# Kernel tuning notes

Hardware: AMD Instinct MI355X
Metric: run time of the kernel (lower is better)

Reference implementation:

```python
import jax, jax.numpy as jnp
import numpy as np

B, N, MODEL_D = 2, 1024, 2048
KQ_D, V_D, H, I = 128, 128, 8, 4
ROPE_THETA = 10000.0


def _rope(x, theta):
    # x: [b, n, ..., d]; positions along axis 1, rotation over last dim d.
    d = x.shape[-1]
    n = x.shape[1]
    inv_freq = theta ** (-jnp.arange(0, d, 2, dtype=jnp.float32) / d)  # [d/2]
    ang = jnp.arange(n, dtype=jnp.float32)[:, None] * inv_freq          # [n, d/2]
    bshape = (1, n) + (1,) * (x.ndim - 3) + (d // 2,)
    cos = jnp.cos(ang).reshape(bshape).astype(x.dtype)
    sin = jnp.sin(ang).reshape(bshape).astype(x.dtype)
    x1, x2 = jnp.split(x, 2, axis=-1)
    return jnp.concatenate([x1 * cos - x2 * sin, x1 * sin + x2 * cos], axis=-1)


def setup_inputs() -> dict:
    key = jax.random.key(0)
    kx, kq, kk, kv, ko = jax.random.split(key, 5)
    s_in = 1.0 / np.sqrt(MODEL_D)
    s_out = 1.0 / np.sqrt(H * I * V_D)
    x = jax.random.normal(kx, (B, N, MODEL_D), jnp.float32)
    Wq = jax.random.normal(kq, (MODEL_D, H, I, KQ_D), jnp.float32) * s_in
    Wk = jax.random.normal(kk, (MODEL_D, H, KQ_D), jnp.float32) * s_in
    Wv = jax.random.normal(kv, (MODEL_D, H, V_D), jnp.float32) * s_in
    Wo = jax.random.normal(ko, (H, I, V_D, MODEL_D), jnp.float32) * s_out
    return {"x": x, "Wq": Wq, "Wk": Wk, "Wv": Wv, "Wo": Wo}


def reference(x, Wq, Wk, Wv, Wo):
    # GQA projections (per Ueajsum specs)
    q = jnp.einsum('bnd,dhik->bnhik', x, Wq)   # [B,N,H,I,K]
    k = jnp.einsum('bnd,dhc->bnhc', x, Wk)     # [B,N,H,K]
    v = jnp.einsum('bnd,dhv->bnhv', x, Wv)     # [B,N,H,V]
    # RoPE on q and k
    q = _rope(q, ROPE_THETA)
    k = _rope(k, ROPE_THETA)
    # Causal softmax attention, each kv head serves I query heads
    scale = 1.0 / np.sqrt(KQ_D)
    scores = jnp.einsum('bnhic,bmhc->bhinm', q, k) * scale  # [B,H,I,N,N]
    n = x.shape[1]
    causal = jnp.tril(jnp.ones((n, n), dtype=bool))
    scores = jnp.where(causal, scores, jnp.finfo(scores.dtype).min)
    p = jax.nn.softmax(scores, axis=-1)
    out = jnp.einsum('bhinm,bmhv->bnhiv', p, v)              # [B,N,H,I,V]
    return jnp.einsum('bnhiv,hivd->bnd', out, Wo)            # [B,N,D]
```

## Files before the change

kernel.cpp:

```cpp
#include <hip/hip_runtime.h>
#include <hip/hip_bf16.h>

typedef __bf16 bf16x8 __attribute__((ext_vector_type(8)));
typedef float floatx4 __attribute__((ext_vector_type(4)));

static __device__ __forceinline__ void async_cp16(const __bf16* g, __bf16* l) {
    typedef const __attribute__((address_space(1))) unsigned int gu32;
    typedef __attribute__((address_space(3))) unsigned int lu32;
    __builtin_amdgcn_global_load_lds((gu32*)g, (lu32*)l, 16, 0, 0);
}

static __device__ __forceinline__ void tile64_f32(
    const float* __restrict__ src, __bf16* __restrict__ dst,
    int R, int C, int r0, int c0, int tid, __bf16* t )
{
    {
        const int r = tid >> 2, cq = (tid & 3) * 16;
        const float* p = src + (size_t)(r0 + r) * C + c0 + cq;
        float4 f0 = *(const float4*)(p);
        float4 f1 = *(const float4*)(p + 4);
        float4 f2 = *(const float4*)(p + 8);
        float4 f3 = *(const float4*)(p + 12);
        __bf16 v[16] = {
            (__bf16)f0.x, (__bf16)f0.y, (__bf16)f0.z, (__bf16)f0.w,
            (__bf16)f1.x, (__bf16)f1.y, (__bf16)f1.z, (__bf16)f1.w,
            (__bf16)f2.x, (__bf16)f2.y, (__bf16)f2.z, (__bf16)f2.w,
            (__bf16)f3.x, (__bf16)f3.y, (__bf16)f3.z, (__bf16)f3.w };
        #pragma unroll
        for (int e = 0; e < 16; ++e) t[(cq + e) * 72 + r] = v[e];
    }
    __syncthreads();
    {
        const int c = tid >> 2, rq = (tid & 3) * 16;
        uint4 u0 = *(const uint4*)(&t[c * 72 + rq]);
        uint4 u1 = *(const uint4*)(&t[c * 72 + rq + 8]);
        __bf16* q = dst + (size_t)(c0 + c) * R + r0 + rq;
        *(uint4*)(q)     = u0;
        *(uint4*)(q + 8) = u1;
    }
}

static __device__ __forceinline__ void tile64_b16(
    const __bf16* __restrict__ src, __bf16* __restrict__ dst,
    int src_ld, int dst_ld, int tid, __bf16* t )
{
    {
        const int r = tid >> 2, cq = (tid & 3) * 16;
        const __bf16* p = src + (size_t)r * src_ld + cq;
        union { uint4 u; __bf16 b[8]; } a0, a1;
        a0.u = *(const uint4*)(p);
        a1.u = *(const uint4*)(p + 8);
        #pragma unroll
        for (int e = 0; e < 8; ++e) {
            t[(cq + e) * 72 + r]     = a0.b[e];
            t[(cq + 8 + e) * 72 + r] = a1.b[e];
        }
    }
    __syncthreads();
    {
        const int c = tid >> 2, rq = (tid & 3) * 16;
        uint4 u0 = *(const uint4*)(&t[c * 72 + rq]);
        uint4 u1 = *(const uint4*)(&t[c * 72 + rq + 8]);
        __bf16* q = dst + (size_t)c * dst_ld + rq;
        *(uint4*)(q)     = u0;
        *(uint4*)(q + 8) = u1;
    }
}

__global__ __launch_bounds__(256) void prep_kernel(
    const float* __restrict__ x,  __bf16* __restrict__ xb,
    const float* __restrict__ Wq, const float* __restrict__ Wk,
    const float* __restrict__ Wv, __bf16* __restrict__ Wt)
{
    __shared__ __bf16 t[64 * 72];
    const int bk  = blockIdx.x;
    const int tid = threadIdx.x;

    if (bk < 2048) {
        int ct = bk & 63, rt = bk >> 6;
        tile64_f32(Wq, Wt, 2048, 4096, rt * 64, ct * 64, tid, t);
    } else if (bk < 2560) {
        int idx = bk - 2048, ct = idx & 15, rt = idx >> 4;
        tile64_f32(Wk, Wt + (size_t)4096 * 2048, 2048, 1024, rt * 64, ct * 64, tid, t);
    } else if (bk < 3072) {
        int idx = bk - 2560, ct = idx & 15, rt = idx >> 4;
        tile64_f32(Wv, Wt + (size_t)5120 * 2048, 2048, 1024, rt * 64, ct * 64, tid, t);
    } else {
        int idx = (bk - 3072) * 256 + tid;
        const float* p = x + (size_t)idx * 8;
        float4 f0 = *(const float4*)p;
        float4 f1 = *(const float4*)(p + 4);
        union { uint4 u; __bf16 b[8]; } o;
        o.b[0] = (__bf16)f0.x; o.b[1] = (__bf16)f0.y; o.b[2] = (__bf16)f0.z; o.b[3] = (__bf16)f0.w;
        o.b[4] = (__bf16)f1.x; o.b[5] = (__bf16)f1.y; o.b[6] = (__bf16)f1.z; o.b[7] = (__bf16)f1.w;
        *(uint4*)(xb + (size_t)idx * 8) = o.u;
    }
}

__global__ __launch_bounds__(256) void rope_vtrans_wot_kernel(
    __bf16* __restrict__ qkv, __bf16* __restrict__ vt,
    const float* __restrict__ Wo, __bf16* __restrict__ WoT)
{
    __shared__ __bf16 t[64 * 72];
    const int bk  = blockIdx.x;
    const int tid = threadIdx.x;

    if (bk < 2560) {
        int idx  = bk * 256 + tid;
        int part = idx & 7;
        int tt   = idx >> 3;
        int head = tt % 40;
        int row  = tt / 40;
        int n    = row & 1023;
        int col0 = (head < 32) ? head * 128 : 4096 + (head - 32) * 128;
        size_t base = (size_t)row * 6144 + col0 + part * 8;

        union { uint4 u; __bf16 b[8]; } x1, x2, o1, o2;
        x1.u = *(const uint4*)(qkv + base);
        x2.u = *(const uint4*)(qkv + base + 64);
        #pragma unroll
        for (int e = 0; e < 8; ++e) {
            int j = part * 8 + e;
            float inv_freq = exp2f(-(float)j * 0.20762050593046015f);
            float ang = (float)n * inv_freq;
            float sv, cv;
            __sincosf(ang, &sv, &cv);
            float a = (float)x1.b[e], b2 = (float)x2.b[e];
            o1.b[e] = (__bf16)(a * cv - b2 * sv);
            o2.b[e] = (__bf16)(a * sv + b2 * cv);
        }
        *(uint4*)(qkv + base)      = o1.u;
        *(uint4*)(qkv + base + 64) = o2.u;
    } else if (bk < 3072) {
        int idx = bk - 2560;
        int bh = idx >> 5, rem = idx & 31;
        int k0 = (rem >> 1) * 64, v0 = (rem & 1) * 64;
        int b = bh >> 3, h = bh & 7;
        const __bf16* src = qkv + (size_t)(b * 1024 + k0) * 6144 + 5120 + h * 128 + v0;
        __bf16* dst = vt + ((size_t)bh * 128 + v0) * 1024 + k0;
        tile64_b16(src, dst, 6144, 1024, tid, t);
    } else {
        int idx = bk - 3072;
        int ct = idx & 31, rt = idx >> 5;
        tile64_f32(Wo, WoT, 4096, 2048, rt * 64, ct * 64, tid, t);
    }
}

__global__ __launch_bounds__(256) void gemm_bt(
    const __bf16* __restrict__ A,
    const __bf16* __restrict__ Bt,
    __bf16* __restrict__ C,
    int M, int lda, int ldb, int ldc,
    int kc_base, int kc_extra)
{
    __shared__ __bf16 As[128 * 64];
    __shared__ __bf16 Bs[128 * 64];

    const int tid  = threadIdx.x;
    const int wave = tid >> 6;
    const int lane = tid & 63;
    const int quad = lane >> 4;
    const int l15  = lane & 15;
    const int wr   = wave >> 1, wc = wave & 1;

    const int bm = blockIdx.y * 128;
    const int bn = blockIdx.x * 128;
    const int z  = blockIdx.z;
    const int Kc = kc_base + ((z == (int)gridDim.z - 1) ? kc_extra : 0);

    A  += (size_t)z * kc_base;
    Bt += (size_t)z * kc_base;
    C  += (size_t)z * M * ldc;

    floatx4 acc[16];
    #pragma unroll
    for (int i = 0; i < 16; ++i) acc[i] = floatx4{0.f, 0.f, 0.f, 0.f};

    const int sr = lane >> 3;
    const int sc = ((lane & 7) ^ sr) * 8;
    const __bf16* a0 = A  + (size_t)(bm + wave * 32 + sr) * lda + sc;
    const __bf16* b0 = Bt + (size_t)(bn + wave * 32 + sr) * ldb + sc;
    __bf16* asd = As + (wave * 32) * 64;
    __bf16* bsd = Bs + (wave * 32) * 64;

    for (int k0 = 0; k0 < Kc; k0 += 64) {
        __syncthreads();
        #pragma unroll
        for (int r = 0; r < 4; ++r) {
            async_cp16(a0 + (size_t)(r * 8) * lda + k0, asd + (r * 8) * 64);
            async_cp16(b0 + (size_t)(r * 8) * ldb + k0, bsd + (r * 8) * 64);
        }
        __syncthreads();

        #pragma unroll
        for (int ko = 0; ko < 2; ++ko) {
            bf16x8 af[4], bf[4];
            #pragma unroll
            for (int t = 0; t < 4; ++t)
                af[t] = *(const bf16x8*)(
                    &As[(wr * 64 + t * 16 + l15) * 64 + (((ko * 4 + quad) ^ (l15 & 7)) * 8)]);
            #pragma unroll
            for (int u = 0; u < 4; ++u)
                bf[u] = *(const bf16x8*)(
                    &Bs[(wc * 64 + u * 16 + l15) * 64 + (((ko * 4 + quad) ^ (l15 & 7)) * 8)]);
            #pragma unroll
            for (int t = 0; t < 4; ++t)
                #pragma unroll
                for (int u = 0; u < 4; ++u)
                    acc[t * 4 + u] = __builtin_amdgcn_mfma_f32_16x16x32_bf16(
                        af[t], bf[u], acc[t * 4 + u], 0, 0, 0);
        }
    }

    #pragma unroll
    for (int t = 0; t < 4; ++t)
        #pragma unroll
        for (int u = 0; u < 4; ++u)
            #pragma unroll
            for (int r = 0; r < 4; ++r) {
                int row = bm + wr * 64 + t * 16 + quad * 4 + r;
                int col = bn + wc * 64 + u * 16 + l15;
                C[(size_t)row * ldc + col] = (__bf16)acc[t * 4 + u][r];
            }
}

__global__ __launch_bounds__(256) void reduce_kernel(
    const __bf16* __restrict__ part, float* __restrict__ out)
{
    int idx = blockIdx.x * 256 + threadIdx.x;
    const size_t S = (size_t)2048 * 2048;
    union { uint4 u; __bf16 b[8]; } p0, p1, p2;
    p0.u = *(const uint4*)(part + (size_t)idx * 8);
    p1.u = *(const uint4*)(part + S + (size_t)idx * 8);
    p2.u = *(const uint4*)(part + 2 * S + (size_t)idx * 8);
    float4 o0, o1;
    o0.x = (float)p0.b[0] + (float)p1.b[0] + (float)p2.b[0];
    o0.y = (float)p0.b[1] + (float)p1.b[1] + (float)p2.b[1];
    o0.z = (float)p0.b[2] + (float)p1.b[2] + (float)p2.b[2];
    o0.w = (float)p0.b[3] + (float)p1.b[3] + (float)p2.b[3];
    o1.x = (float)p0.b[4] + (float)p1.b[4] + (float)p2.b[4];
    o1.y = (float)p0.b[5] + (float)p1.b[5] + (float)p2.b[5];
    o1.z = (float)p0.b[6] + (float)p1.b[6] + (float)p2.b[6];
    o1.w = (float)p0.b[7] + (float)p1.b[7] + (float)p2.b[7];
    *(float4*)(out + (size_t)idx * 8)     = o0;
    *(float4*)(out + (size_t)idx * 8 + 4) = o1;
}

__global__ __launch_bounds__(512, 2) void attn_kernel(
    const __bf16* __restrict__ qkv,
    const __bf16* __restrict__ vt,
    __bf16* __restrict__ ao)
{
    const int PS_LD = 72;
    __shared__ __bf16 Ks[64 * 128];
    __shared__ __bf16 Vs[128 * 64];
    __shared__ __bf16 Ps[8][16 * PS_LD];

    const int tid  = threadIdx.x;
    const int wave = tid >> 6;
    const int lane = tid & 63;
    const int quad = lane >> 4;
    const int l15  = lane & 15;
    const int i    = wave >> 1;
    const int rt   = wave & 1;

    const int pair = blockIdx.x;
    const int bh   = blockIdx.y;
    const int b    = bh >> 3, h = bh & 7;
    const __bf16* vtb = vt + (size_t)bh * 128 * 1024;

    const int keyA = wave * 8 + (lane >> 4);
    const int keyB = keyA + 4;
    const int chA  = (lane & 15) ^ (keyA & 15);
    const int chB  = (lane & 15) ^ (keyB & 15);
    const __bf16* gK0 = qkv + (size_t)(b * 1024 + keyA) * 6144 + 4096 + h * 128 + chA * 8;
    const __bf16* gK1 = qkv + (size_t)(b * 1024 + keyB) * 6144 + 4096 + h * 128 + chB * 8;
    __bf16* lK0 = Ks + (wave * 8) * 128;
    __bf16* lK1 = Ks + (wave * 8 + 4) * 128;

    const int vdA = wave * 16 + (lane >> 3);
    const int vdB = vdA + 8;
    const int cvA = (lane & 7) ^ (vdA & 7);
    const int cvB = (lane & 7) ^ (vdB & 7);
    const __bf16* gV0 = vtb + (size_t)vdA * 1024 + cvA * 8;
    const __bf16* gV1 = vtb + (size_t)vdB * 1024 + cvB * 8;
    __bf16* lV0 = Vs + (wave * 16) * 64;
    __bf16* lV1 = Vs + (wave * 16 + 8) * 64;

    bf16x8 onesf;
    #pragma unroll
    for (int j = 0; j < 8; ++j) onesf[j] = (__bf16)1.0f;

    const float C2 = 0.12751898549f;

    #pragma unroll
    for (int ph = 0; ph < 2; ++ph) {
        const int qt    = ph ? (31 - pair) : pair;
        const int qrow0 = qt * 32 + rt * 16;

        const __bf16* qp = qkv + (size_t)(b * 1024 + qrow0 + l15) * 6144 + (h * 4 + i) * 128;
        bf16x8 qf[4];
        #pragma unroll
        for (int c = 0; c < 4; ++c)
            qf[c] = *(const bf16x8*)(qp + c * 32 + quad * 8);

        floatx4 acc[8];
        #pragma unroll
        for (int u = 0; u < 8; ++u) acc[u] = floatx4{0.f, 0.f, 0.f, 0.f};
        floatx4 accl = floatx4{0.f, 0.f, 0.f, 0.f};

        const int ntiles = (qt >> 1) + 1;
        for (int t = 0; t < ntiles; ++t) {
            const int kt = t * 64;
            __syncthreads();
            async_cp16(gK0 + (size_t)kt * 6144, lK0);
            async_cp16(gK1 + (size_t)kt * 6144, lK1);
            async_cp16(gV0 + kt, lV0);
            async_cp16(gV1 + kt, lV1);
            __syncthreads();

            floatx4 s[4];
            #pragma unroll
            for (int ks = 0; ks < 4; ++ks) s[ks] = floatx4{0.f, 0.f, 0.f, 0.f};
            #pragma unroll
            for (int c = 0; c < 4; ++c) {
                #pragma unroll
                for (int ks = 0; ks < 4; ++ks) {
                    bf16x8 kf = *(const bf16x8*)(
                        &Ks[(ks * 16 + l15) * 128 + ((c * 4 + quad) ^ l15) * 8]);
                    s[ks] = __builtin_amdgcn_mfma_f32_16x16x32_bf16(qf[c], kf, s[ks], 0, 0, 0);
                }
            }

            #pragma unroll
            for (int r = 0; r < 4; ++r) {
                int qrow = qrow0 + quad * 4 + r;
                #pragma unroll
                for (int ks = 0; ks < 4; ++ks) {
                    int kc = kt + ks * 16 + l15;
                    float p = (kc <= qrow) ? exp2f(s[ks][r] * C2) : 0.0f;
                    Ps[wave][(quad * 4 + r) * PS_LD + ks * 16 + l15] = (__bf16)p;
                }
            }

            #pragma unroll
            for (int s2 = 0; s2 < 2; ++s2) {
                bf16x8 pa = *(const bf16x8*)(&Ps[wave][l15 * PS_LD + s2 * 32 + quad * 8]);
                accl = __builtin_amdgcn_mfma_f32_16x16x32_bf16(pa, onesf, accl, 0, 0, 0);
                #pragma unroll
                for (int u = 0; u < 8; ++u) {
                    bf16x8 vf = *(const bf16x8*)(
                        &Vs[(u * 16 + l15) * 64 + (((s2 * 4 + quad) ^ (l15 & 7))) * 8]);
                    acc[u] = __builtin_amdgcn_mfma_f32_16x16x32_bf16(pa, vf, acc[u], 0, 0, 0);
                }
            }
        }

        #pragma unroll
        for (int r = 0; r < 4; ++r) {
            float inv = 1.0f / accl[r];
            int row = qrow0 + quad * 4 + r;
            __bf16* op = ao + (size_t)(b * 1024 + row) * 4096 + (h * 4 + i) * 128;
            #pragma unroll
            for (int u = 0; u < 8; ++u)
                op[u * 16 + l15] = (__bf16)(acc[u][r] * inv);
        }
    }
}

extern "C" void kernel_launch(void* const* d_in, const int* in_sizes, int n_in,
                              void* d_out, int out_size, void* d_ws, size_t ws_size,
                              hipStream_t stream)
{
    const float* x  = (const float*)d_in[0];
    const float* Wq = (const float*)d_in[1];
    const float* Wk = (const float*)d_in[2];
    const float* Wv = (const float*)d_in[3];
    const float* Wo = (const float*)d_in[4];
    float* out = (float*)d_out;

    const size_t MB = 1024 * 1024;
    char* ws = (char*)d_ws;
    __bf16* qkv  = (__bf16*)(ws);
    __bf16* vtb  = (__bf16*)(ws + 24 * MB);
    __bf16* xb   = (__bf16*)(ws + 28 * MB);
    __bf16* Wt   = (__bf16*)(ws + 36 * MB);
    __bf16* WoT  = (__bf16*)(ws + 28 * MB);
    __bf16* ao   = (__bf16*)(ws + 44 * MB);
    __bf16* part = (__bf16*)(ws);

    prep_kernel<<<5120, 256, 0, stream>>>(x, xb, Wq, Wk, Wv, Wt);
    gemm_bt<<<dim3(48, 16), 256, 0, stream>>>(xb, Wt, qkv, 2048, 2048, 2048, 6144, 2048, 0);
    rope_vtrans_wot_kernel<<<5120, 256, 0, stream>>>(qkv, vtb, Wo, WoT);
    attn_kernel<<<dim3(16, 16), 512, 0, stream>>>(qkv, vtb, ao);
    gemm_bt<<<dim3(16, 16, 3), 256, 0, stream>>>(ao, WoT, part, 2048, 4096, 4096, 2048, 1344, 64);
    reduce_kernel<<<2048, 256, 0, stream>>>(part, out);
}
```

Measured before the change: 295.5 us.

## Rework bf16 GEMM into 256x256 ping-pong pipelined tiles with 512 threads

The shared GEMM now uses 256x256 output tiles computed by 8 waves, with double-buffered LDS. The next K-slice's A and B tiles are prefetched asynchronously across four interleaved MFMA phases, separated by barriers and s_setprio. The goal is to overlap global-to-LDS copies with matrix math and to reuse each loaded tile more. The cost is fewer blocks (192 for both GEMMs), which leaves some CUs idle. Each block also needs 128KB of LDS and many accumulator registers, so occupancy is limited to one block per CU.

```diff
diff --git a/kernel.cpp b/kernel.cpp
--- a/kernel.cpp
+++ b/kernel.cpp
@@ -146,82 +146,190 @@
     }
 }
 
-__global__ __launch_bounds__(256) void gemm_bt(
+__global__ __launch_bounds__(512) void gemm_bt(
     const __bf16* __restrict__ A,
     const __bf16* __restrict__ Bt,
     __bf16* __restrict__ C,
     int M, int lda, int ldb, int ldc,
     int kc_base, int kc_extra)
 {
-    __shared__ __bf16 As[128 * 64];
-    __shared__ __bf16 Bs[128 * 64];
+    __shared__ __bf16 As[2][256 * 64];
+    __shared__ __bf16 Bs[2][256 * 64];
 
     const int tid  = threadIdx.x;
     const int wave = tid >> 6;
     const int lane = tid & 63;
     const int quad = lane >> 4;
     const int l15  = lane & 15;
-    const int wr   = wave >> 1, wc = wave & 1;
-
-    const int bm = blockIdx.y * 128;
-    const int bn = blockIdx.x * 128;
+    const int wr   = wave >> 2;
+    const int wc   = wave & 3;
+
+    const int bm = blockIdx.y * 256;
+    const int bn = blockIdx.x * 256;
     const int z  = blockIdx.z;
     const int Kc = kc_base + ((z == (int)gridDim.z - 1) ? kc_extra : 0);
+    const int NT = Kc >> 6;
 
     A  += (size_t)z * kc_base;
     Bt += (size_t)z * kc_base;
     C  += (size_t)z * M * ldc;
 
-    floatx4 acc[16];
+    floatx4 acc[32];
     #pragma unroll
-    for (int i = 0; i < 16; ++i) acc[i] = floatx4{0.f, 0.f, 0.f, 0.f};
+    for (int i = 0; i < 32; ++i) acc[i] = floatx4{0.f, 0.f, 0.f, 0.f};
 
     const int sr = lane >> 3;
     const int sc = ((lane & 7) ^ sr) * 8;
-    const __bf16* a0 = A  + (size_t)(bm + wave * 32 + sr) * lda + sc;
-    const __bf16* b0 = Bt + (size_t)(bn + wave * 32 + sr) * ldb + sc;
-    __bf16* asd = As + (wave * 32) * 64;
-    __bf16* bsd = Bs + (wave * 32) * 64;
-
-    for (int k0 = 0; k0 < Kc; k0 += 64) {
-        __syncthreads();
-        #pragma unroll
-        for (int r = 0; r < 4; ++r) {
-            async_cp16(a0 + (size_t)(r * 8) * lda + k0, asd + (r * 8) * 64);
-            async_cp16(b0 + (size_t)(r * 8) * ldb + k0, bsd + (r * 8) * 64);
-        }
-        __syncthreads();
-
-        #pragma unroll
-        for (int ko = 0; ko < 2; ++ko) {
-            bf16x8 af[4], bf[4];
-            #pragma unroll
-            for (int t = 0; t < 4; ++t)
-                af[t] = *(const bf16x8*)(
-                    &As[(wr * 64 + t * 16 + l15) * 64 + (((ko * 4 + quad) ^ (l15 & 7)) * 8)]);
-            #pragma unroll
-            for (int u = 0; u < 4; ++u)
-                bf[u] = *(const bf16x8*)(
-                    &Bs[(wc * 64 + u * 16 + l15) * 64 + (((ko * 4 + quad) ^ (l15 & 7)) * 8)]);
-            #pragma unroll
-            for (int t = 0; t < 4; ++t)
-                #pragma unroll
-                for (int u = 0; u < 4; ++u)
-                    acc[t * 4 + u] = __builtin_amdgcn_mfma_f32_16x16x32_bf16(
-                        af[t], bf[u], acc[t * 4 + u], 0, 0, 0);
-        }
-    }
+    const __bf16* a0 = A  + (size_t)(bm + wave * 8 + sr) * lda + sc;
+    const __bf16* b0 = Bt + (size_t)(bn + wave * 8 + sr) * ldb + sc;
+    const int ldsw = wave * 512;
+
+    const int arow = (wr * 128 + l15) * 64;
+    const int brow = (wc * 64  + l15) * 64;
+    const int cx0  = ((0 + quad) ^ (l15 & 7)) * 8;
+    const int cx1  = ((4 + quad) ^ (l15 & 7)) * 8;
 
     #pragma unroll
-    for (int t = 0; t < 4; ++t)
-        #pragma unroll
-        for (int u = 0; u < 4; ++u)
-            #pragma unroll
-            for (int r = 0; r < 4; ++r) {
-                int row = bm + wr * 64 + t * 16 + quad * 4 + r;
-                int col = bn + wc * 64 + u * 16 + l15;
-                C[(size_t)row * ldc + col] = (__bf16)acc[t * 4 + u][r];
-            }
+    for (int q = 0; q < 4; ++q)
+        async_cp16(a0 + (size_t)(q * 64) * lda, (__bf16*)&As[0][q * 4096 + ldsw]);
+    #pragma unroll
+    for (int q = 0; q < 4; ++q)
+        async_cp16(b0 + (size_t)(q * 64) * ldb, (__bf16*)&Bs[0][q * 4096 + ldsw]);
+    if (NT > 1) {
+        #pragma unroll
+        for (int q = 0; q < 4; ++q)
+            async_cp16(b0 + (size_t)(q * 64) * ldb + 64, (__bf16*)&Bs[1][q * 4096 + ldsw]);
+        asm volatile("s_waitcnt vmcnt(4)" ::: "memory");
+    } else {
+        asm volatile("s_waitcnt vmcnt(0)" ::: "memory");
+    }
+    __builtin_amdgcn_s_barrier();
+    __builtin_amdgcn_sched_barrier(0);
+
+    for (int t = 0; t < NT; ++t) {
+        const int cur = t & 1;
+        const __bf16* Ac = As[cur];
+        const __bf16* Bc = Bs[cur];
+        __bf16* An = (__bf16*)As[cur ^ 1];
+        __bf16* Bn = (__bf16*)Bs[cur];
+
+        bf16x8 af[4][2], bfA[2][2], bfB[2][2];
+
+        #pragma unroll
+        for (int tt = 0; tt < 4; ++tt) {
+            af[tt][0] = *(const bf16x8*)(&Ac[arow + tt * 1024 + cx0]);
+            af[tt][1] = *(const bf16x8*)(&Ac[arow + tt * 1024 + cx1]);
+        }
+        #pragma unroll
+        for (int uu = 0; uu < 2; ++uu) {
+            bfA[uu][0] = *(const bf16x8*)(&Bc[brow + uu * 1024 + cx0]);
+            bfA[uu][1] = *(const bf16x8*)(&Bc[brow + uu * 1024 + cx1]);
+        }
+        if (t + 1 < NT) {
+            #pragma unroll
+            for (int q = 0; q < 4; ++q)
+                async_cp16(a0 + (size_t)(q * 64) * lda + (t + 1) * 64,
+                           An + q * 4096 + ldsw);
+        }
+        __builtin_amdgcn_s_barrier();
+        asm volatile("s_waitcnt lgkmcnt(0)" ::: "memory");
+        __builtin_amdgcn_sched_barrier(0);
+        __builtin_amdgcn_s_setprio(1);
+        #pragma unroll
+        for (int ko = 0; ko < 2; ++ko)
+            #pragma unroll
+            for (int tt = 0; tt < 4; ++tt)
+                #pragma unroll
+                for (int uu = 0; uu < 2; ++uu)
+                    acc[tt * 4 + uu] = __builtin_amdgcn_mfma_f32_16x16x32_bf16(
+                        af[tt][ko], bfA[uu][ko], acc[tt * 4 + uu], 0, 0, 0);
+        __builtin_amdgcn_s_setprio(0);
+        __builtin_amdgcn_s_barrier();
+        __builtin_amdgcn_sched_barrier(0);
+
+        #pragma unroll
+        for (int uu = 0; uu < 2; ++uu) {
+            bfB[uu][0] = *(const bf16x8*)(&Bc[brow + (2 + uu) * 1024 + cx0]);
+            bfB[uu][1] = *(const bf16x8*)(&Bc[brow + (2 + uu) * 1024 + cx1]);
+        }
+        __builtin_amdgcn_s_barrier();
+        asm volatile("s_waitcnt lgkmcnt(0)" ::: "memory");
+        __builtin_amdgcn_sched_barrier(0);
+        __builtin_amdgcn_s_setprio(1);
+        #pragma unroll
+        for (int ko = 0; ko < 2; ++ko)
+            #pragma unroll
+            for (int tt = 0; tt < 4; ++tt)
+                #pragma unroll
+                for (int uu = 0; uu < 2; ++uu)
+                    acc[tt * 4 + 2 + uu] = __builtin_amdgcn_mfma_f32_16x16x32_bf16(
+                        af[tt][ko], bfB[uu][ko], acc[tt * 4 + 2 + uu], 0, 0, 0);
+        __builtin_amdgcn_s_setprio(0);
+        __builtin_amdgcn_s_barrier();
+        __builtin_amdgcn_sched_barrier(0);
+
+        #pragma unroll
+        for (int tt = 0; tt < 4; ++tt) {
+            af[tt][0] = *(const bf16x8*)(&Ac[arow + (4 + tt) * 1024 + cx0]);
+            af[tt][1] = *(const bf16x8*)(&Ac[arow + (4 + tt) * 1024 + cx1]);
+        }
+        if (t + 2 < NT) {
+            #pragma unroll
+            for (int q = 0; q < 2; ++q)
+                async_cp16(b0 + (size_t)(q * 64) * ldb + (t + 2) * 64,
+                           Bn + q * 4096 + ldsw);
+        }
+        __builtin_amdgcn_s_barrier();
+        asm volatile("s_waitcnt lgkmcnt(0)" ::: "memory");
+        __builtin_amdgcn_sched_barrier(0);
+        __builtin_amdgcn_s_setprio(1);
+        #pragma unroll
+        for (int ko = 0; ko < 2; ++ko)
+            #pragma unroll
+            for (int tt = 0; tt < 4; ++tt)
+                #pragma unroll
+                for (int uu = 0; uu < 2; ++uu)
+                    acc[(4 + tt) * 4 + uu] = __builtin_amdgcn_mfma_f32_16x16x32_bf16(
+                        af[tt][ko], bfA[uu][ko], acc[(4 + tt) * 4 + uu], 0, 0, 0);
+        __builtin_amdgcn_s_setprio(0);
+        __builtin_amdgcn_s_barrier();
+        __builtin_amdgcn_sched_barrier(0);
+
+        if (t + 2 < NT) {
+            #pragma unroll
+            for (int q = 2; q < 4; ++q)
+                async_cp16(b0 + (size_t)(q * 64) * ldb + (t + 2) * 64,
+                           Bn + q * 4096 + ldsw);
+        }
+        __builtin_amdgcn_s_setprio(1);
+        #pragma unroll
+        for (int ko = 0; ko < 2; ++ko)
+            #pragma unroll
+            for (int tt = 0; tt < 4; ++tt)
+                #pragma unroll
+                for (int uu = 0; uu < 2; ++uu)
+                    acc[(4 + tt) * 4 + 2 + uu] = __builtin_amdgcn_mfma_f32_16x16x32_bf16(
+                        af[tt][ko], bfB[uu][ko], acc[(4 + tt) * 4 + 2 + uu], 0, 0, 0);
+        __builtin_amdgcn_s_setprio(0);
+        if (t + 2 < NT) {
+            asm volatile("s_waitcnt vmcnt(4)" ::: "memory");
+        } else {
+            asm volatile("s_waitcnt vmcnt(0)" ::: "memory");
+        }
+        __builtin_amdgcn_s_barrier();
+        __builtin_amdgcn_sched_barrier(0);
+    }
+
+    #pragma unroll
+    for (int tt = 0; tt < 8; ++tt)
+        #pragma unroll
+        for (int uu = 0; uu < 4; ++uu) {
+            const int row = bm + wr * 128 + tt * 16 + quad * 4;
+            const int col = bn + wc * 64 + uu * 16 + l15;
+            #pragma unroll
+            for (int r = 0; r < 4; ++r)
+                C[(size_t)(row + r) * ldc + col] = (__bf16)acc[tt * 4 + uu][r];
+        }
 }
 
 __global__ __launch_bounds__(256) void reduce_kernel(
@@ -390,9 +498,9 @@
     __bf16* part = (__bf16*)(ws);
 
     prep_kernel<<<5120, 256, 0, stream>>>(x, xb, Wq, Wk, Wv, Wt);
-    gemm_bt<<<dim3(48, 16), 256, 0, stream>>>(xb, Wt, qkv, 2048, 2048, 2048, 6144, 2048, 0);
+    gemm_bt<<<dim3(24, 8), 512, 0, stream>>>(xb, Wt, qkv, 2048, 2048, 2048, 6144, 2048, 0);
     rope_vtrans_wot_kernel<<<5120, 256, 0, stream>>>(qkv, vtb, Wo, WoT);
     attn_kernel<<<dim3(16, 16), 512, 0, stream>>>(qkv, vtb, ao);
-    gemm_bt<<<dim3(16, 16, 3), 256, 0, stream>>>(ao, WoT, part, 2048, 4096, 4096, 2048, 1344, 64);
+    gemm_bt<<<dim3(8, 8, 3), 512, 0, stream>>>(ao, WoT, part, 2048, 4096, 4096, 2048, 1344, 64);
     reduce_kernel<<<2048, 256, 0, stream>>>(part, out);
 }
```

After: 295.1 us. No clear change (-0.1%).
